# Optimization experiments

Measured on AMD Instinct MI355X. Metric: run time of the kernel, lower is better.

## Reference

```python
import jax, jax.numpy as jnp
import numpy as np


def _gcn_conv(x, edge_index, W, b):
    """Standard PyG GCNConv: add self-loops, symmetric normalization, x@W, scatter-add, +bias."""
    n = x.shape[0]
    loop = jnp.arange(n, dtype=edge_index.dtype)
    src = jnp.concatenate([edge_index[0], loop])  # [E+N]
    dst = jnp.concatenate([edge_index[1], loop])  # [E+N]
    # degree of destination nodes (unit edge weights + self loops)
    deg = jax.ops.segment_sum(jnp.ones_like(dst, dtype=x.dtype), dst, num_segments=n)
    dinv = jnp.where(deg > 0, jax.lax.rsqrt(deg), 0.0)
    norm = dinv[src] * dinv[dst]  # [E+N]
    h = x @ W  # [N, C_out] -- transform before aggregation (fewer bytes moved)
    msg = h[src] * norm[:, None]  # gather + scale
    out = jax.ops.segment_sum(msg, dst, num_segments=n)  # scatter-add
    return out + b


def setup_inputs() -> dict:
    key = jax.random.key(0)
    k1, k2, k3, k4 = jax.random.split(key, 4)
    N, E, C_in, C_hid, C_out = 50000, 800000, 64, 64, 40
    x = jax.random.normal(k1, (N, C_in), dtype=jnp.float32)
    edge_index = jax.random.randint(k2, (2, E), 0, N, dtype=jnp.int64)
    # Glorot-ish init for weights, zeros for biases (PyG GCNConv default)
    W1 = jax.random.normal(k3, (C_in, C_hid), dtype=jnp.float32) * (1.0 / np.sqrt(C_in))
    b1 = jnp.zeros((C_hid,), dtype=jnp.float32)
    W2 = jax.random.normal(k4, (C_hid, C_out), dtype=jnp.float32) * (1.0 / np.sqrt(C_hid))
    b2 = jnp.zeros((C_out,), dtype=jnp.float32)
    return {"x": x, "edge_index": edge_index, "W1": W1, "b1": b1, "W2": W2, "b2": b2}


def reference(x, edge_index, W1, b1, W2, b2):
    h = jax.nn.relu(_gcn_conv(x, edge_index, W1, b1))
    # F.dropout(training=False) is identity in eval mode
    h = _gcn_conv(h, edge_index, W2, b2)
    return jax.nn.log_softmax(h, axis=1)
```

## Files before the change

### kernel.cpp

```cpp
#include <hip/hip_runtime.h>
#include <hip/hip_fp16.h>
#include <math.h>


#define SHIFT   9
#define RPB     512
#define NBMAX   128
#define SLACK   16384
#define CHUNK_P 2048

__global__ void k_init(int* __restrict__ bcur, int nb) {
    int t = threadIdx.x;
    if (t < nb) bcur[t] = t * SLACK;
}

__global__ void k_part_gemm(const long long* __restrict__ ei64,
                            const int* __restrict__ ei32,
                            int* __restrict__ bcur,
                            unsigned int* __restrict__ ebkt, int E, int nb,
                            int npart,
                            const float* __restrict__ x,
                            const float* __restrict__ W1,
                            __half* __restrict__ hs1, int n) {
    __shared__ __align__(16) float smem[2 * 64 * 68];
    if ((int)blockIdx.x < npart) {
        int* cnt   = (int*)smem;
        int* rbase = cnt + NBMAX;
        int* is64p = rbase + NBMAX;
        int t = threadIdx.x;
        if (t < NBMAX) cnt[t] = 0;
        if (t == 0) {
            int is64 = 1;
            for (int i = 0; i < 64; ++i)
                if (ei32[2 * i + 1] != 0) { is64 = 0; break; }
            *is64p = is64;
        }
        __syncthreads();
        int is64 = *is64p;
        int lo = blockIdx.x * CHUNK_P;
        int hi = lo + CHUNK_P; if (hi > E) hi = E;
        for (int e = lo + t; e < hi; e += 256) {
            int d = is64 ? (int)ei64[E + e] : ei32[E + e];
            atomicAdd(&cnt[d >> SHIFT], 1);
        }
        __syncthreads();
        for (int b = t; b < nb; b += 256) {
            int c = cnt[b];
            rbase[b] = c ? atomicAdd(&bcur[b], c) : 0;
            cnt[b] = 0;
        }
        __syncthreads();
        for (int e = lo + t; e < hi; e += 256) {
            int s, d;
            if (is64) { s = (int)ei64[e]; d = (int)ei64[E + e]; }
            else      { s = ei32[e];      d = ei32[E + e]; }
            int b = d >> SHIFT;
            int pos = rbase[b] + atomicAdd(&cnt[b], 1);
            ebkt[pos] = ((unsigned int)(d & (RPB - 1)) << 16) | (unsigned int)s;
        }
    } else {
        float* Wl = smem;
        float* Xl = smem + 64 * 68;
        int t  = threadIdx.x;
        int tr = t >> 4, tc = t & 15;
        int base = (blockIdx.x - npart) * 64;

        for (int i = t; i < 64 * 17; i += 256) {
            int k = i / 17, c4 = (i % 17) * 4;
            float4 w = make_float4(0.f, 0.f, 0.f, 0.f);
            if (c4 < 64) w = *(const float4*)&W1[k * 64 + c4];
            *(float4*)&Wl[k * 68 + c4] = w;
        }
        for (int rr = tr; rr < 64; rr += 16) {
            int row = base + rr; if (row >= n) row = n - 1;
            float4 v = *(const float4*)&x[(size_t)row * 64 + tc * 4];
            Xl[(tc * 4 + 0) * 68 + rr] = v.x;
            Xl[(tc * 4 + 1) * 68 + rr] = v.y;
            Xl[(tc * 4 + 2) * 68 + rr] = v.z;
            Xl[(tc * 4 + 3) * 68 + rr] = v.w;
        }
        __syncthreads();

        float acc[4][4] = {{0.f}};
#pragma unroll 8
        for (int k = 0; k < 64; ++k) {
            float4 xv = *(const float4*)&Xl[k * 68 + tr * 4];
            float4 wv = *(const float4*)&Wl[k * 68 + tc * 4];
            acc[0][0] = fmaf(xv.x, wv.x, acc[0][0]);
            acc[0][1] = fmaf(xv.x, wv.y, acc[0][1]);
            acc[0][2] = fmaf(xv.x, wv.z, acc[0][2]);
            acc[0][3] = fmaf(xv.x, wv.w, acc[0][3]);
            acc[1][0] = fmaf(xv.y, wv.x, acc[1][0]);
            acc[1][1] = fmaf(xv.y, wv.y, acc[1][1]);
            acc[1][2] = fmaf(xv.y, wv.z, acc[1][2]);
            acc[1][3] = fmaf(xv.y, wv.w, acc[1][3]);
            acc[2][0] = fmaf(xv.z, wv.x, acc[2][0]);
            acc[2][1] = fmaf(xv.z, wv.y, acc[2][1]);
            acc[2][2] = fmaf(xv.z, wv.z, acc[2][2]);
            acc[2][3] = fmaf(xv.z, wv.w, acc[2][3]);
            acc[3][0] = fmaf(xv.w, wv.x, acc[3][0]);
            acc[3][1] = fmaf(xv.w, wv.y, acc[3][1]);
            acc[3][2] = fmaf(xv.w, wv.z, acc[3][2]);
            acc[3][3] = fmaf(xv.w, wv.w, acc[3][3]);
        }
#pragma unroll
        for (int i = 0; i < 4; ++i) {
            int r = base + tr * 4 + i;
            if (r >= n) break;
            __half2 p0 = __floats2half2_rn(acc[i][0], acc[i][1]);
            __half2 p1 = __floats2half2_rn(acc[i][2], acc[i][3]);
            *(__half2*)&hs1[(size_t)r * 64 + tc * 4]     = p0;
            *(__half2*)&hs1[(size_t)r * 64 + tc * 4 + 2] = p1;
        }
    }
}

__global__ void k_build(const unsigned int* __restrict__ ebkt,
                        const int* __restrict__ bcur,
                        int* __restrict__ row_beg, int* __restrict__ row_end,
                        float* __restrict__ dinv,
                        unsigned short* __restrict__ csr_src, int N) {
    __shared__ int cnt[RPB];
    __shared__ int wsum[256];
    int t = threadIdx.x, b = blockIdx.x;
    int rows0 = b << SHIFT;
    int nrows = N - rows0; if (nrows > RPB) nrows = RPB;
    for (int i = t; i < RPB; i += 256) cnt[i] = 0;
    __syncthreads();
    int lo = b * SLACK, hi = bcur[b];
    for (int e = lo + t; e < hi; e += 256)
        atomicAdd(&cnt[ebkt[e] >> 16], 1);
    __syncthreads();
    int i0 = 2 * t, i1 = 2 * t + 1;
    int c0 = cnt[i0], c1 = cnt[i1];
    wsum[t] = c0 + c1;
    __syncthreads();
    for (int off = 1; off < 256; off <<= 1) {
        int u = (t >= off) ? wsum[t - off] : 0;
        __syncthreads();
        wsum[t] += u;
        __syncthreads();
    }
    int beg0 = lo + ((t == 0) ? 0 : wsum[t - 1]);
    int beg1 = beg0 + c0;
    cnt[i0] = beg0;
    cnt[i1] = beg1;
    if (i0 < nrows) {
        row_beg[rows0 + i0] = beg0; row_end[rows0 + i0] = beg0 + c0;
        dinv[rows0 + i0] = rsqrtf((float)c0 + 1.0f);
    }
    if (i1 < nrows) {
        row_beg[rows0 + i1] = beg1; row_end[rows0 + i1] = beg1 + c1;
        dinv[rows0 + i1] = rsqrtf((float)c1 + 1.0f);
    }
    __syncthreads();
    for (int e = lo + t; e < hi; e += 256) {
        unsigned int v = ebkt[e];
        int pos = atomicAdd(&cnt[v >> 16], 1);
        csr_src[pos] = (unsigned short)(v & 0xffffu);
    }
}

template<int COUT>
__global__ void k_gemm(const __half* __restrict__ xin,
                       const float* __restrict__ W,
                       const float* __restrict__ dinv,
                       __half* __restrict__ hs, int n) {
    __shared__ float Wl[64 * 68];
    __shared__ float Xl[64 * 68];
    int t  = threadIdx.x;
    int tr = t >> 4, tc = t & 15;
    int base = blockIdx.x * 64;

    for (int i = t; i < 64 * 17; i += 256) {
        int k = i / 17, c4 = (i % 17) * 4;
        float4 w = make_float4(0.f, 0.f, 0.f, 0.f);
        if (c4 < COUT) w = *(const float4*)&W[k * COUT + c4];
        *(float4*)&Wl[k * 68 + c4] = w;
    }
    for (int rr = tr; rr < 64; rr += 16) {
        int row = base + rr; if (row >= n) row = n - 1;
        uint2 u = *(const uint2*)&xin[(size_t)row * 64 + tc * 4];
        float2 a = __half22float2(*(__half2*)&u.x);
        float2 c = __half22float2(*(__half2*)&u.y);
        Xl[(tc * 4 + 0) * 68 + rr] = a.x;
        Xl[(tc * 4 + 1) * 68 + rr] = a.y;
        Xl[(tc * 4 + 2) * 68 + rr] = c.x;
        Xl[(tc * 4 + 3) * 68 + rr] = c.y;
    }
    __syncthreads();

    float acc[4][4] = {{0.f}};
#pragma unroll 8
    for (int k = 0; k < 64; ++k) {
        float4 xv = *(const float4*)&Xl[k * 68 + tr * 4];
        float4 wv = *(const float4*)&Wl[k * 68 + tc * 4];
        acc[0][0] = fmaf(xv.x, wv.x, acc[0][0]);
        acc[0][1] = fmaf(xv.x, wv.y, acc[0][1]);
        acc[0][2] = fmaf(xv.x, wv.z, acc[0][2]);
        acc[0][3] = fmaf(xv.x, wv.w, acc[0][3]);
        acc[1][0] = fmaf(xv.y, wv.x, acc[1][0]);
        acc[1][1] = fmaf(xv.y, wv.y, acc[1][1]);
        acc[1][2] = fmaf(xv.y, wv.z, acc[1][2]);
        acc[1][3] = fmaf(xv.y, wv.w, acc[1][3]);
        acc[2][0] = fmaf(xv.z, wv.x, acc[2][0]);
        acc[2][1] = fmaf(xv.z, wv.y, acc[2][1]);
        acc[2][2] = fmaf(xv.z, wv.z, acc[2][2]);
        acc[2][3] = fmaf(xv.z, wv.w, acc[2][3]);
        acc[3][0] = fmaf(xv.w, wv.x, acc[3][0]);
        acc[3][1] = fmaf(xv.w, wv.y, acc[3][1]);
        acc[3][2] = fmaf(xv.w, wv.z, acc[3][2]);
        acc[3][3] = fmaf(xv.w, wv.w, acc[3][3]);
    }
#pragma unroll
    for (int i = 0; i < 4; ++i) {
        int r = base + tr * 4 + i;
        if (r >= n) break;
        float dv = dinv[r];
        __half2 p0 = __floats2half2_rn(acc[i][0] * dv, acc[i][1] * dv);
        __half2 p1 = __floats2half2_rn(acc[i][2] * dv, acc[i][3] * dv);
        if (tc * 4 + 3 < COUT) {
            *(__half2*)&hs[(size_t)r * COUT + tc * 4]     = p0;
            *(__half2*)&hs[(size_t)r * COUT + tc * 4 + 2] = p1;
        }
    }
}

__global__ void k_gather_relu64(const __half* __restrict__ hs,
                                const int* __restrict__ rbg,
                                const int* __restrict__ ren,
                                const unsigned short* __restrict__ ci,
                                const float* __restrict__ dinv,
                                const float* __restrict__ bias,
                                __half* __restrict__ out, int n) {
    int row = blockIdx.x * 4 + (threadIdx.x >> 6);
    if (row >= n) return;
    int lane = threadIdx.x & 63;
    int g = lane >> 3, q = lane & 7;
    int beg = rbg[row], end = ren[row];

    float4 aa = make_float4(0.f, 0.f, 0.f, 0.f);
    float4 ab = make_float4(0.f, 0.f, 0.f, 0.f);
    for (int base = beg; base < end; base += 64) {
        int mm = end - base; if (mm > 64) mm = 64;
        int idx = (lane < mm) ? (int)ci[base + lane] : 0;
        for (int j = 0; 8 * j < mm; ++j) {
            int e = 8 * j + g;
            int s = __shfl(idx, e, 64);
            if (base + e < end) {
                float ds = dinv[s];
                uint4 u = ((const uint4*)(hs + ((size_t)s << 6)))[q];
                float2 f0 = __half22float2(*(__half2*)&u.x);
                float2 f1 = __half22float2(*(__half2*)&u.y);
                float2 f2 = __half22float2(*(__half2*)&u.z);
                float2 f3 = __half22float2(*(__half2*)&u.w);
                aa.x = fmaf(f0.x, ds, aa.x); aa.y = fmaf(f0.y, ds, aa.y);
                aa.z = fmaf(f1.x, ds, aa.z); aa.w = fmaf(f1.y, ds, aa.w);
                ab.x = fmaf(f2.x, ds, ab.x); ab.y = fmaf(f2.y, ds, ab.y);
                ab.z = fmaf(f3.x, ds, ab.z); ab.w = fmaf(f3.y, ds, ab.w);
            }
        }
    }
#pragma unroll
    for (int o = 8; o < 64; o <<= 1) {
        aa.x += __shfl_xor(aa.x, o, 64); aa.y += __shfl_xor(aa.y, o, 64);
        aa.z += __shfl_xor(aa.z, o, 64); aa.w += __shfl_xor(aa.w, o, 64);
        ab.x += __shfl_xor(ab.x, o, 64); ab.y += __shfl_xor(ab.y, o, 64);
        ab.z += __shfl_xor(ab.z, o, 64); ab.w += __shfl_xor(ab.w, o, 64);
    }
    float dv = dinv[row];
    uint4 su = ((const uint4*)(hs + ((size_t)row << 6)))[q];
    float2 s0 = __half22float2(*(__half2*)&su.x);
    float2 s1 = __half22float2(*(__half2*)&su.y);
    float2 s2 = __half22float2(*(__half2*)&su.z);
    float2 s3 = __half22float2(*(__half2*)&su.w);
    float4 bv0 = *(const float4*)&bias[q * 8];
    float4 bv1 = *(const float4*)&bias[q * 8 + 4];
    float v0 = fmaxf((aa.x + s0.x * dv) * dv + bv0.x, 0.f);
    float v1 = fmaxf((aa.y + s0.y * dv) * dv + bv0.y, 0.f);
    float v2 = fmaxf((aa.z + s1.x * dv) * dv + bv0.z, 0.f);
    float v3 = fmaxf((aa.w + s1.y * dv) * dv + bv0.w, 0.f);
    float v4 = fmaxf((ab.x + s2.x * dv) * dv + bv1.x, 0.f);
    float v5 = fmaxf((ab.y + s2.y * dv) * dv + bv1.y, 0.f);
    float v6 = fmaxf((ab.z + s3.x * dv) * dv + bv1.z, 0.f);
    float v7 = fmaxf((ab.w + s3.y * dv) * dv + bv1.w, 0.f);
    if (lane < 8) {
        uint4 st;
        ((__half2*)&st)[0] = __floats2half2_rn(v0, v1);
        ((__half2*)&st)[1] = __floats2half2_rn(v2, v3);
        ((__half2*)&st)[2] = __floats2half2_rn(v4, v5);
        ((__half2*)&st)[3] = __floats2half2_rn(v6, v7);
        ((uint4*)(out + ((size_t)row << 6)))[q] = st;
    }
}

__global__ void k_gather_lsm40(const __half* __restrict__ hs,
                               const int* __restrict__ rbg,
                               const int* __restrict__ ren,
                               const unsigned short* __restrict__ ci,
                               const float* __restrict__ dinv,
                               const float* __restrict__ bias,
                               float* __restrict__ out, int n) {
    int row = blockIdx.x * 4 + (threadIdx.x >> 6);
    if (row >= n) return;
    int lane = threadIdx.x & 63;
    int g = lane >> 4, q = lane & 15;
    int beg = rbg[row], end = ren[row];

    uint2 selfu = make_uint2(0u, 0u);
    if (q < 10)
        selfu = ((const uint2*)(hs + (size_t)row * 40))[q];

    float4 a = make_float4(0.f, 0.f, 0.f, 0.f);
    for (int base = beg; base < end; base += 64) {
        int mm = end - base; if (mm > 64) mm = 64;
        int idx = (lane < mm) ? (int)ci[base + lane] : 0;
        for (int j = 0; 4 * j < mm; ++j) {
            int s = __shfl(idx, 4 * j + g, 64);
            if (q < 10 && base + 4 * j + g < end) {
                uint2 u = ((const uint2*)(hs + (size_t)s * 40))[q];
                float2 f0 = __half22float2(*(__half2*)&u.x);
                float2 f1 = __half22float2(*(__half2*)&u.y);
                a.x += f0.x; a.y += f0.y; a.z += f1.x; a.w += f1.y;
            }
        }
    }
    a.x += __shfl_xor(a.x, 16, 64); a.y += __shfl_xor(a.y, 16, 64);
    a.z += __shfl_xor(a.z, 16, 64); a.w += __shfl_xor(a.w, 16, 64);
    a.x += __shfl_xor(a.x, 32, 64); a.y += __shfl_xor(a.y, 32, 64);
    a.z += __shfl_xor(a.z, 32, 64); a.w += __shfl_xor(a.w, 32, 64);

    float2 s0 = __half22float2(*(__half2*)&selfu.x);
    float2 s1 = __half22float2(*(__half2*)&selfu.y);
    float dv = dinv[row];
    float v0 = -INFINITY, v1 = -INFINITY, v2 = -INFINITY, v3 = -INFINITY;
    if (q < 10) {
        float4 bv = *(const float4*)&bias[q * 4];
        v0 = (a.x + s0.x) * dv + bv.x;
        v1 = (a.y + s0.y) * dv + bv.y;
        v2 = (a.z + s1.x) * dv + bv.z;
        v3 = (a.w + s1.y) * dv + bv.w;
    }
    float mx = fmaxf(fmaxf(v0, v1), fmaxf(v2, v3));
#pragma unroll
    for (int o = 1; o < 16; o <<= 1) mx = fmaxf(mx, __shfl_xor(mx, o, 64));
    float e0 = (q < 10) ? expf(v0 - mx) : 0.f;
    float e1 = (q < 10) ? expf(v1 - mx) : 0.f;
    float e2 = (q < 10) ? expf(v2 - mx) : 0.f;
    float e3 = (q < 10) ? expf(v3 - mx) : 0.f;
    float sm = (e0 + e1) + (e2 + e3);
#pragma unroll
    for (int o = 1; o < 16; o <<= 1) sm += __shfl_xor(sm, o, 64);
    if (lane < 16 && q < 10) {
        float ls = logf(sm);
        float4 r = make_float4(v0 - mx - ls, v1 - mx - ls,
                               v2 - mx - ls, v3 - mx - ls);
        *(float4*)&out[(size_t)row * 40 + q * 4] = r;
    }
}

extern "C" void kernel_launch(void* const* d_in, const int* in_sizes, int n_in,
                              void* d_out, int out_size, void* d_ws, size_t ws_size,
                              hipStream_t stream) {
    const float* x  = (const float*)d_in[0];
    const void*  ei = d_in[1];
    const float* W1 = (const float*)d_in[2];
    const float* b1 = (const float*)d_in[3];
    const float* W2 = (const float*)d_in[4];
    const float* b2 = (const float*)d_in[5];
    float* out = (float*)d_out;

    const int C_IN = 64;
    const int N = in_sizes[0] / C_IN;
    const int E = in_sizes[1] / 2;
    (void)n_in; (void)out_size; (void)ws_size;

    char* ws = (char*)d_ws;
    size_t off = 0;
    auto alloc = [&](size_t bytes) -> void* {
        void* p = ws + off;
        off += (bytes + 255) & ~(size_t)255;
        return p;
    };
    int*            bcur    = (int*)           alloc(NBMAX * 4);
    unsigned int*   ebkt    = (unsigned int*)  alloc((size_t)NBMAX * SLACK * 4);
    unsigned short* csr_src = (unsigned short*)alloc((size_t)NBMAX * SLACK * 2);
    int*            row_beg = (int*)           alloc((size_t)N * 4);
    int*            row_end = (int*)           alloc((size_t)N * 4);
    float*          dinv    = (float*)         alloc((size_t)N * 4);
    __half*         hs1     = (__half*)        alloc((size_t)N * 64 * 2);
    __half*         h1b     = (__half*)        alloc((size_t)N * 64 * 2);
    __half*         hs2     = (__half*)        alloc((size_t)N * 40 * 2);

    const int nb    = (N + RPB - 1) >> SHIFT;
    const int ngrid = (N + 63) / 64;
    const int npart = (E + CHUNK_P - 1) / CHUNK_P;

    k_init<<<1, 128, 0, stream>>>(bcur, nb);
    k_part_gemm<<<npart + ngrid, 256, 0, stream>>>(
        (const long long*)ei, (const int*)ei, bcur, ebkt, E, nb, npart,
        x, W1, hs1, N);
    k_build<<<nb, 256, 0, stream>>>(ebkt, bcur, row_beg, row_end, dinv,
                                    csr_src, N);
    k_gather_relu64<<<(N + 3) / 4, 256, 0, stream>>>(
        hs1, row_beg, row_end, csr_src, dinv, b1, h1b, N);
    k_gemm<40><<<ngrid, 256, 0, stream>>>(h1b, W2, dinv, hs2, N);
    k_gather_lsm40<<<(N + 3) / 4, 256, 0, stream>>>(
        hs2, row_beg, row_end, csr_src, dinv, b2, out, N);
}
```

Measured before the change: 113.9 us.

## Fuse layer-1 gather/ReLU with layer-2 GEMM into one kernel

Merges the first-layer neighbor aggregation plus bias/ReLU with the second-layer 64x40 GEMM. Each block gathers 64 rows (8 waves × 8 rows each) into shared memory, then 160 threads run the GEMM and write scaled fp16 results. This removes the h1b intermediate write and read and one kernel launch. In exchange each wave now handles 8 rows serially, there are fewer blocks (N/64), and only 160 of 512 threads are active during the GEMM phase, which can reduce parallelism and latency hiding in the gather.

New measurement: 123.3 us. 1.08x slower.

```diff
diff --git a/kernel.cpp b/kernel.cpp
--- a/kernel.cpp
+++ b/kernel.cpp
@@ -161,136 +161,127 @@
     }
 }
 
-template<int COUT>
-__global__ void k_gemm(const __half* __restrict__ xin,
-                       const float* __restrict__ W,
-                       const float* __restrict__ dinv,
-                       __half* __restrict__ hs, int n) {
-    __shared__ float Wl[64 * 68];
+__global__ __launch_bounds__(512, 4)
+void k_gather_gemm2(const __half* __restrict__ hs,
+                    const float* __restrict__ W,
+                    const int* __restrict__ rbg,
+                    const int* __restrict__ ren,
+                    const unsigned short* __restrict__ ci,
+                    const float* __restrict__ dinv,
+                    const float* __restrict__ bias,
+                    __half* __restrict__ hs2,
+                    int n) {
     __shared__ float Xl[64 * 68];
-    int t  = threadIdx.x;
-    int tr = t >> 4, tc = t & 15;
+    __shared__ float Wl[64 * 44];
+    int t = threadIdx.x;
     int base = blockIdx.x * 64;
 
-    for (int i = t; i < 64 * 17; i += 256) {
-        int k = i / 17, c4 = (i % 17) * 4;
+    for (int i = t; i < 64 * 11; i += 512) {
+        int k = i / 11, c4 = (i % 11) * 4;
         float4 w = make_float4(0.f, 0.f, 0.f, 0.f);
-        if (c4 < COUT) w = *(const float4*)&W[k * COUT + c4];
-        *(float4*)&Wl[k * 68 + c4] = w;
-    }
-    for (int rr = tr; rr < 64; rr += 16) {
-        int row = base + rr; if (row >= n) row = n - 1;
-        uint2 u = *(const uint2*)&xin[(size_t)row * 64 + tc * 4];
-        float2 a = __half22float2(*(__half2*)&u.x);
-        float2 c = __half22float2(*(__half2*)&u.y);
-        Xl[(tc * 4 + 0) * 68 + rr] = a.x;
-        Xl[(tc * 4 + 1) * 68 + rr] = a.y;
-        Xl[(tc * 4 + 2) * 68 + rr] = c.x;
-        Xl[(tc * 4 + 3) * 68 + rr] = c.y;
-    }
-    __syncthreads();
-
-    float acc[4][4] = {{0.f}};
+        if (c4 < 40) w = *(const float4*)&W[k * 40 + c4];
+        *(float4*)&Wl[k * 44 + c4] = w;
+    }
+
+    int w    = t >> 6;
+    int lane = t & 63;
+    int g = lane >> 3, q = lane & 7;
+
+    for (int it = 0; it < 8; ++it) {
+        int row = base + w * 8 + it;
+        if (row >= n) break;
+        int beg = rbg[row], end = ren[row];
+
+        float4 aa = make_float4(0.f, 0.f, 0.f, 0.f);
+        float4 ab = make_float4(0.f, 0.f, 0.f, 0.f);
+        for (int eb = beg; eb < end; eb += 64) {
+            int mm = end - eb; if (mm > 64) mm = 64;
+            int idx = (lane < mm) ? (int)ci[eb + lane] : 0;
+            for (int j = 0; 8 * j < mm; ++j) {
+                int e = 8 * j + g;
+                int s = __shfl(idx, e, 64);
+                if (eb + e < end) {
+                    float ds = dinv[s];
+                    uint4 u = ((const uint4*)(hs + ((size_t)s << 6)))[q];
+                    float2 f0 = __half22float2(*(__half2*)&u.x);
+                    float2 f1 = __half22float2(*(__half2*)&u.y);
+                    float2 f2 = __half22float2(*(__half2*)&u.z);
+                    float2 f3 = __half22float2(*(__half2*)&u.w);
+                    aa.x = fmaf(f0.x, ds, aa.x); aa.y = fmaf(f0.y, ds, aa.y);
+                    aa.z = fmaf(f1.x, ds, aa.z); aa.w = fmaf(f1.y, ds, aa.w);
+                    ab.x = fmaf(f2.x, ds, ab.x); ab.y = fmaf(f2.y, ds, ab.y);
+                    ab.z = fmaf(f3.x, ds, ab.z); ab.w = fmaf(f3.y, ds, ab.w);
+                }
+            }
+        }
+#pragma unroll
+        for (int o = 8; o < 64; o <<= 1) {
+            aa.x += __shfl_xor(aa.x, o, 64); aa.y += __shfl_xor(aa.y, o, 64);
+            aa.z += __shfl_xor(aa.z, o, 64); aa.w += __shfl_xor(aa.w, o, 64);
+            ab.x += __shfl_xor(ab.x, o, 64); ab.y += __shfl_xor(ab.y, o, 64);
+            ab.z += __shfl_xor(ab.z, o, 64); ab.w += __shfl_xor(ab.w, o, 64);
+        }
+        float dv = dinv[row];
+        uint4 su = ((const uint4*)(hs + ((size_t)row << 6)))[q];
+        float2 s0 = __half22float2(*(__half2*)&su.x);
+        float2 s1 = __half22float2(*(__half2*)&su.y);
+        float2 s2 = __half22float2(*(__half2*)&su.z);
+        float2 s3 = __half22float2(*(__half2*)&su.w);
+        float4 bv0 = *(const float4*)&bias[q * 8];
+        float4 bv1 = *(const float4*)&bias[q * 8 + 4];
+        float v0 = fmaxf((aa.x + s0.x * dv) * dv + bv0.x, 0.f);
+        float v1 = fmaxf((aa.y + s0.y * dv) * dv + bv0.y, 0.f);
+        float v2 = fmaxf((aa.z + s1.x * dv) * dv + bv0.z, 0.f);
+        float v3 = fmaxf((aa.w + s1.y * dv) * dv + bv0.w, 0.f);
+        float v4 = fmaxf((ab.x + s2.x * dv) * dv + bv1.x, 0.f);
+        float v5 = fmaxf((ab.y + s2.y * dv) * dv + bv1.y, 0.f);
+        float v6 = fmaxf((ab.z + s3.x * dv) * dv + bv1.z, 0.f);
+        float v7 = fmaxf((ab.w + s3.y * dv) * dv + bv1.w, 0.f);
+        float s01 = (g & 1) ? v1 : v0;
+        float s23 = (g & 1) ? v3 : v2;
+        float s45 = (g & 1) ? v5 : v4;
+        float s67 = (g & 1) ? v7 : v6;
+        float s03 = (g & 2) ? s23 : s01;
+        float s47 = (g & 2) ? s67 : s45;
+        float val = (g & 4) ? s47 : s03;
+        Xl[(q * 8 + g) * 68 + (row - base)] = val;
+    }
+    __syncthreads();
+
+    if (t < 256 && (t & 15) < 10) {
+        int tr = t >> 4, tc = t & 15;
+        float acc[4][4] = {{0.f}};
 #pragma unroll 8
-    for (int k = 0; k < 64; ++k) {
-        float4 xv = *(const float4*)&Xl[k * 68 + tr * 4];
-        float4 wv = *(const float4*)&Wl[k * 68 + tc * 4];
-        acc[0][0] = fmaf(xv.x, wv.x, acc[0][0]);
-        acc[0][1] = fmaf(xv.x, wv.y, acc[0][1]);
-        acc[0][2] = fmaf(xv.x, wv.z, acc[0][2]);
-        acc[0][3] = fmaf(xv.x, wv.w, acc[0][3]);
-        acc[1][0] = fmaf(xv.y, wv.x, acc[1][0]);
-        acc[1][1] = fmaf(xv.y, wv.y, acc[1][1]);
-        acc[1][2] = fmaf(xv.y, wv.z, acc[1][2]);
-        acc[1][3] = fmaf(xv.y, wv.w, acc[1][3]);
-        acc[2][0] = fmaf(xv.z, wv.x, acc[2][0]);
-        acc[2][1] = fmaf(xv.z, wv.y, acc[2][1]);
-        acc[2][2] = fmaf(xv.z, wv.z, acc[2][2]);
-        acc[2][3] = fmaf(xv.z, wv.w, acc[2][3]);
-        acc[3][0] = fmaf(xv.w, wv.x, acc[3][0]);
-        acc[3][1] = fmaf(xv.w, wv.y, acc[3][1]);
-        acc[3][2] = fmaf(xv.w, wv.z, acc[3][2]);
-        acc[3][3] = fmaf(xv.w, wv.w, acc[3][3]);
-    }
-#pragma unroll
-    for (int i = 0; i < 4; ++i) {
-        int r = base + tr * 4 + i;
-        if (r >= n) break;
-        float dv = dinv[r];
-        __half2 p0 = __floats2half2_rn(acc[i][0] * dv, acc[i][1] * dv);
-        __half2 p1 = __floats2half2_rn(acc[i][2] * dv, acc[i][3] * dv);
-        if (tc * 4 + 3 < COUT) {
-            *(__half2*)&hs[(size_t)r * COUT + tc * 4]     = p0;
-            *(__half2*)&hs[(size_t)r * COUT + tc * 4 + 2] = p1;
-        }
-    }
-}
-
-__global__ void k_gather_relu64(const __half* __restrict__ hs,
-                                const int* __restrict__ rbg,
-                                const int* __restrict__ ren,
-                                const unsigned short* __restrict__ ci,
-                                const float* __restrict__ dinv,
-                                const float* __restrict__ bias,
-                                __half* __restrict__ out, int n) {
-    int row = blockIdx.x * 4 + (threadIdx.x >> 6);
-    if (row >= n) return;
-    int lane = threadIdx.x & 63;
-    int g = lane >> 3, q = lane & 7;
-    int beg = rbg[row], end = ren[row];
-
-    float4 aa = make_float4(0.f, 0.f, 0.f, 0.f);
-    float4 ab = make_float4(0.f, 0.f, 0.f, 0.f);
-    for (int base = beg; base < end; base += 64) {
-        int mm = end - base; if (mm > 64) mm = 64;
-        int idx = (lane < mm) ? (int)ci[base + lane] : 0;
-        for (int j = 0; 8 * j < mm; ++j) {
-            int e = 8 * j + g;
-            int s = __shfl(idx, e, 64);
-            if (base + e < end) {
-                float ds = dinv[s];
-                uint4 u = ((const uint4*)(hs + ((size_t)s << 6)))[q];
-                float2 f0 = __half22float2(*(__half2*)&u.x);
-                float2 f1 = __half22float2(*(__half2*)&u.y);
-                float2 f2 = __half22float2(*(__half2*)&u.z);
-                float2 f3 = __half22float2(*(__half2*)&u.w);
-                aa.x = fmaf(f0.x, ds, aa.x); aa.y = fmaf(f0.y, ds, aa.y);
-                aa.z = fmaf(f1.x, ds, aa.z); aa.w = fmaf(f1.y, ds, aa.w);
-                ab.x = fmaf(f2.x, ds, ab.x); ab.y = fmaf(f2.y, ds, ab.y);
-                ab.z = fmaf(f3.x, ds, ab.z); ab.w = fmaf(f3.y, ds, ab.w);
-            }
-        }
-    }
-#pragma unroll
-    for (int o = 8; o < 64; o <<= 1) {
-        aa.x += __shfl_xor(aa.x, o, 64); aa.y += __shfl_xor(aa.y, o, 64);
-        aa.z += __shfl_xor(aa.z, o, 64); aa.w += __shfl_xor(aa.w, o, 64);
-        ab.x += __shfl_xor(ab.x, o, 64); ab.y += __shfl_xor(ab.y, o, 64);
-        ab.z += __shfl_xor(ab.z, o, 64); ab.w += __shfl_xor(ab.w, o, 64);
-    }
-    float dv = dinv[row];
-    uint4 su = ((const uint4*)(hs + ((size_t)row << 6)))[q];
-    float2 s0 = __half22float2(*(__half2*)&su.x);
-    float2 s1 = __half22float2(*(__half2*)&su.y);
-    float2 s2 = __half22float2(*(__half2*)&su.z);
-    float2 s3 = __half22float2(*(__half2*)&su.w);
-    float4 bv0 = *(const float4*)&bias[q * 8];
-    float4 bv1 = *(const float4*)&bias[q * 8 + 4];
-    float v0 = fmaxf((aa.x + s0.x * dv) * dv + bv0.x, 0.f);
-    float v1 = fmaxf((aa.y + s0.y * dv) * dv + bv0.y, 0.f);
-    float v2 = fmaxf((aa.z + s1.x * dv) * dv + bv0.z, 0.f);
-    float v3 = fmaxf((aa.w + s1.y * dv) * dv + bv0.w, 0.f);
-    float v4 = fmaxf((ab.x + s2.x * dv) * dv + bv1.x, 0.f);
-    float v5 = fmaxf((ab.y + s2.y * dv) * dv + bv1.y, 0.f);
-    float v6 = fmaxf((ab.z + s3.x * dv) * dv + bv1.z, 0.f);
-    float v7 = fmaxf((ab.w + s3.y * dv) * dv + bv1.w, 0.f);
-    if (lane < 8) {
-        uint4 st;
-        ((__half2*)&st)[0] = __floats2half2_rn(v0, v1);
-        ((__half2*)&st)[1] = __floats2half2_rn(v2, v3);
-        ((__half2*)&st)[2] = __floats2half2_rn(v4, v5);
-        ((__half2*)&st)[3] = __floats2half2_rn(v6, v7);
-        ((uint4*)(out + ((size_t)row << 6)))[q] = st;
+        for (int k = 0; k < 64; ++k) {
+            float4 xv = *(const float4*)&Xl[k * 68 + tr * 4];
+            float4 wv = *(const float4*)&Wl[k * 44 + tc * 4];
+            acc[0][0] = fmaf(xv.x, wv.x, acc[0][0]);
+            acc[0][1] = fmaf(xv.x, wv.y, acc[0][1]);
+            acc[0][2] = fmaf(xv.x, wv.z, acc[0][2]);
+            acc[0][3] = fmaf(xv.x, wv.w, acc[0][3]);
+            acc[1][0] = fmaf(xv.y, wv.x, acc[1][0]);
+            acc[1][1] = fmaf(xv.y, wv.y, acc[1][1]);
+            acc[1][2] = fmaf(xv.y, wv.z, acc[1][2]);
+            acc[1][3] = fmaf(xv.y, wv.w, acc[1][3]);
+            acc[2][0] = fmaf(xv.z, wv.x, acc[2][0]);
+            acc[2][1] = fmaf(xv.z, wv.y, acc[2][1]);
+            acc[2][2] = fmaf(xv.z, wv.z, acc[2][2]);
+            acc[2][3] = fmaf(xv.z, wv.w, acc[2][3]);
+            acc[3][0] = fmaf(xv.w, wv.x, acc[3][0]);
+            acc[3][1] = fmaf(xv.w, wv.y, acc[3][1]);
+            acc[3][2] = fmaf(xv.w, wv.z, acc[3][2]);
+            acc[3][3] = fmaf(xv.w, wv.w, acc[3][3]);
+        }
+#pragma unroll
+        for (int i = 0; i < 4; ++i) {
+            int r = base + tr * 4 + i;
+            if (r >= n) break;
+            float dvv = dinv[r];
+            __half2 p0 = __floats2half2_rn(acc[i][0] * dvv, acc[i][1] * dvv);
+            __half2 p1 = __floats2half2_rn(acc[i][2] * dvv, acc[i][3] * dvv);
+            *(__half2*)&hs2[(size_t)r * 40 + tc * 4]     = p0;
+            *(__half2*)&hs2[(size_t)r * 40 + tc * 4 + 2] = p1;
+        }
     }
 }
 
@@ -389,7 +380,6 @@
     int*            row_end = (int*)           alloc((size_t)N * 4);
     float*          dinv    = (float*)         alloc((size_t)N * 4);
     __half*         hs1     = (__half*)        alloc((size_t)N * 64 * 2);
-    __half*         h1b     = (__half*)        alloc((size_t)N * 64 * 2);
     __half*         hs2     = (__half*)        alloc((size_t)N * 40 * 2);
 
     const int nb    = (N + RPB - 1) >> SHIFT;
@@ -402,9 +392,8 @@
         x, W1, hs1, N);
     k_build<<<nb, 256, 0, stream>>>(ebkt, bcur, row_beg, row_end, dinv,
                                     csr_src, N);
-    k_gather_relu64<<<(N + 3) / 4, 256, 0, stream>>>(
-        hs1, row_beg, row_end, csr_src, dinv, b1, h1b, N);
-    k_gemm<40><<<ngrid, 256, 0, stream>>>(h1b, W2, dinv, hs2, N);
+    k_gather_gemm2<<<ngrid, 512, 0, stream>>>(
+        hs1, W2, row_beg, row_end, csr_src, dinv, b1, hs2, N);
     k_gather_lsm40<<<(N + 3) / 4, 256, 0, stream>>>(
         hs2, row_beg, row_end, csr_src, dinv, b2, out, N);
 }
```

## Halve bucket size, stash edges in LDS, replace init kernel with memcpy

Applied to the files above, without the earlier changes.

Bucket granularity drops from 512 to 256 rows, which gives 256 buckets so each thread in the build kernel owns one row and the scan is simpler. The partition kernel now reads the edge list once and stashes packed (dst,src) pairs in shared memory, removing the second global read pass. The bucket-cursor init kernel is replaced by a host-to-device async memcpy from a static host array. The gather kernels hoist the self-row and dinv loads earlier. Risks: the memcpy from pageable static memory may synchronise or add latency, and bucket slack of 8192 per 256 rows must still hold the per-bucket edge count.

Result: faster. 106.7 us (-6.3%).

```diff
diff --git a/kernel.cpp b/kernel.cpp
--- a/kernel.cpp
+++ b/kernel.cpp
@@ -3,16 +3,11 @@
 #include <math.h>
 
 
-#define SHIFT   9
-#define RPB     512
-#define NBMAX   128
-#define SLACK   16384
+#define SHIFT   8
+#define RPB     256
+#define NBMAX   256
+#define SLACK   8192
 #define CHUNK_P 2048
-
-__global__ void k_init(int* __restrict__ bcur, int nb) {
-    int t = threadIdx.x;
-    if (t < nb) bcur[t] = t * SLACK;
-}
 
 __global__ void k_part_gemm(const long long* __restrict__ ei64,
                             const int* __restrict__ ei32,
@@ -25,10 +20,11 @@
     __shared__ __align__(16) float smem[2 * 64 * 68];
     if ((int)blockIdx.x < npart) {
         int* cnt   = (int*)smem;
-        int* rbase = cnt + NBMAX;
-        int* is64p = rbase + NBMAX;
+        int* rbase = cnt + 256;
+        int* is64p = rbase + 256;
+        int* stash = is64p + 1;
         int t = threadIdx.x;
-        if (t < NBMAX) cnt[t] = 0;
+        cnt[t] = 0;
         if (t == 0) {
             int is64 = 1;
             for (int i = 0; i < 64; ++i)
@@ -40,23 +36,24 @@
         int lo = blockIdx.x * CHUNK_P;
         int hi = lo + CHUNK_P; if (hi > E) hi = E;
         for (int e = lo + t; e < hi; e += 256) {
-            int d = is64 ? (int)ei64[E + e] : ei32[E + e];
-            atomicAdd(&cnt[d >> SHIFT], 1);
-        }
-        __syncthreads();
-        for (int b = t; b < nb; b += 256) {
-            int c = cnt[b];
-            rbase[b] = c ? atomicAdd(&bcur[b], c) : 0;
-            cnt[b] = 0;
-        }
-        __syncthreads();
-        for (int e = lo + t; e < hi; e += 256) {
             int s, d;
             if (is64) { s = (int)ei64[e]; d = (int)ei64[E + e]; }
             else      { s = ei32[e];      d = ei32[E + e]; }
-            int b = d >> SHIFT;
+            stash[e - lo] = (int)(((unsigned int)d << 16) | (unsigned int)s);
+            atomicAdd(&cnt[d >> SHIFT], 1);
+        }
+        __syncthreads();
+        {
+            int c = cnt[t];
+            rbase[t] = c ? atomicAdd(&bcur[t], c) : 0;
+            cnt[t] = 0;
+        }
+        __syncthreads();
+        for (int e = lo + t; e < hi; e += 256) {
+            unsigned int v = (unsigned int)stash[e - lo];
+            int b = (int)(v >> 16) >> SHIFT;
             int pos = rbase[b] + atomicAdd(&cnt[b], 1);
-            ebkt[pos] = ((unsigned int)(d & (RPB - 1)) << 16) | (unsigned int)s;
+            ebkt[pos] = (((v >> 16) & (RPB - 1)) << 16) | (v & 0xffffu);
         }
     } else {
         float* Wl = smem;
@@ -121,43 +118,105 @@
                         float* __restrict__ dinv,
                         unsigned short* __restrict__ csr_src, int N) {
     __shared__ int cnt[RPB];
-    __shared__ int wsum[256];
+    __shared__ int ssum[RPB];
     int t = threadIdx.x, b = blockIdx.x;
     int rows0 = b << SHIFT;
-    int nrows = N - rows0; if (nrows > RPB) nrows = RPB;
-    for (int i = t; i < RPB; i += 256) cnt[i] = 0;
+    cnt[t] = 0;
     __syncthreads();
     int lo = b * SLACK, hi = bcur[b];
     for (int e = lo + t; e < hi; e += 256)
         atomicAdd(&cnt[ebkt[e] >> 16], 1);
     __syncthreads();
-    int i0 = 2 * t, i1 = 2 * t + 1;
-    int c0 = cnt[i0], c1 = cnt[i1];
-    wsum[t] = c0 + c1;
+    int c = cnt[t];
+    ssum[t] = c;
     __syncthreads();
     for (int off = 1; off < 256; off <<= 1) {
-        int u = (t >= off) ? wsum[t - off] : 0;
-        __syncthreads();
-        wsum[t] += u;
-        __syncthreads();
-    }
-    int beg0 = lo + ((t == 0) ? 0 : wsum[t - 1]);
-    int beg1 = beg0 + c0;
-    cnt[i0] = beg0;
-    cnt[i1] = beg1;
-    if (i0 < nrows) {
-        row_beg[rows0 + i0] = beg0; row_end[rows0 + i0] = beg0 + c0;
-        dinv[rows0 + i0] = rsqrtf((float)c0 + 1.0f);
-    }
-    if (i1 < nrows) {
-        row_beg[rows0 + i1] = beg1; row_end[rows0 + i1] = beg1 + c1;
-        dinv[rows0 + i1] = rsqrtf((float)c1 + 1.0f);
-    }
+        int u = (t >= off) ? ssum[t - off] : 0;
+        __syncthreads();
+        ssum[t] += u;
+        __syncthreads();
+    }
+    int beg = lo + ssum[t] - c;
+    int row = rows0 + t;
+    if (row < N) {
+        row_beg[row] = beg; row_end[row] = beg + c;
+        dinv[row] = rsqrtf((float)c + 1.0f);
+    }
+    cnt[t] = beg;
     __syncthreads();
     for (int e = lo + t; e < hi; e += 256) {
         unsigned int v = ebkt[e];
         int pos = atomicAdd(&cnt[v >> 16], 1);
         csr_src[pos] = (unsigned short)(v & 0xffffu);
+    }
+}
+
+__global__ void k_gather_relu64(const __half* __restrict__ hs,
+                                const int* __restrict__ rbg,
+                                const int* __restrict__ ren,
+                                const unsigned short* __restrict__ ci,
+                                const float* __restrict__ dinv,
+                                const float* __restrict__ bias,
+                                __half* __restrict__ out, int n) {
+    int row = blockIdx.x * 4 + (threadIdx.x >> 6);
+    if (row >= n) return;
+    int lane = threadIdx.x & 63;
+    int g = lane >> 3, q = lane & 7;
+    int beg = rbg[row], end = ren[row];
+
+    float dv = dinv[row];
+    uint4 su = ((const uint4*)(hs + ((size_t)row << 6)))[q];
+
+    float4 aa = make_float4(0.f, 0.f, 0.f, 0.f);
+    float4 ab = make_float4(0.f, 0.f, 0.f, 0.f);
+    for (int base = beg; base < end; base += 64) {
+        int mm = end - base; if (mm > 64) mm = 64;
+        int idx = (lane < mm) ? (int)ci[base + lane] : 0;
+        for (int j = 0; 8 * j < mm; ++j) {
+            int e = 8 * j + g;
+            int s = __shfl(idx, e, 64);
+            if (base + e < end) {
+                float ds = dinv[s];
+                uint4 u = ((const uint4*)(hs + ((size_t)s << 6)))[q];
+                float2 f0 = __half22float2(*(__half2*)&u.x);
+                float2 f1 = __half22float2(*(__half2*)&u.y);
+                float2 f2 = __half22float2(*(__half2*)&u.z);
+                float2 f3 = __half22float2(*(__half2*)&u.w);
+                aa.x = fmaf(f0.x, ds, aa.x); aa.y = fmaf(f0.y, ds, aa.y);
+                aa.z = fmaf(f1.x, ds, aa.z); aa.w = fmaf(f1.y, ds, aa.w);
+                ab.x = fmaf(f2.x, ds, ab.x); ab.y = fmaf(f2.y, ds, ab.y);
+                ab.z = fmaf(f3.x, ds, ab.z); ab.w = fmaf(f3.y, ds, ab.w);
+            }
+        }
+    }
+#pragma unroll
+    for (int o = 8; o < 64; o <<= 1) {
+        aa.x += __shfl_xor(aa.x, o, 64); aa.y += __shfl_xor(aa.y, o, 64);
+        aa.z += __shfl_xor(aa.z, o, 64); aa.w += __shfl_xor(aa.w, o, 64);
+        ab.x += __shfl_xor(ab.x, o, 64); ab.y += __shfl_xor(ab.y, o, 64);
+        ab.z += __shfl_xor(ab.z, o, 64); ab.w += __shfl_xor(ab.w, o, 64);
+    }
+    float2 s0 = __half22float2(*(__half2*)&su.x);
+    float2 s1 = __half22float2(*(__half2*)&su.y);
+    float2 s2 = __half22float2(*(__half2*)&su.z);
+    float2 s3 = __half22float2(*(__half2*)&su.w);
+    float4 bv0 = *(const float4*)&bias[q * 8];
+    float4 bv1 = *(const float4*)&bias[q * 8 + 4];
+    float v0 = fmaxf((aa.x + s0.x * dv) * dv + bv0.x, 0.f);
+    float v1 = fmaxf((aa.y + s0.y * dv) * dv + bv0.y, 0.f);
+    float v2 = fmaxf((aa.z + s1.x * dv) * dv + bv0.z, 0.f);
+    float v3 = fmaxf((aa.w + s1.y * dv) * dv + bv0.w, 0.f);
+    float v4 = fmaxf((ab.x + s2.x * dv) * dv + bv1.x, 0.f);
+    float v5 = fmaxf((ab.y + s2.y * dv) * dv + bv1.y, 0.f);
+    float v6 = fmaxf((ab.z + s3.x * dv) * dv + bv1.z, 0.f);
+    float v7 = fmaxf((ab.w + s3.y * dv) * dv + bv1.w, 0.f);
+    if (lane < 8) {
+        uint4 st;
+        ((__half2*)&st)[0] = __floats2half2_rn(v0, v1);
+        ((__half2*)&st)[1] = __floats2half2_rn(v2, v3);
+        ((__half2*)&st)[2] = __floats2half2_rn(v4, v5);
+        ((__half2*)&st)[3] = __floats2half2_rn(v6, v7);
+        ((uint4*)(out + ((size_t)row << 6)))[q] = st;
     }
 }
 
@@ -226,74 +285,6 @@
     }
 }
 
-__global__ void k_gather_relu64(const __half* __restrict__ hs,
-                                const int* __restrict__ rbg,
-                                const int* __restrict__ ren,
-                                const unsigned short* __restrict__ ci,
-                                const float* __restrict__ dinv,
-                                const float* __restrict__ bias,
-                                __half* __restrict__ out, int n) {
-    int row = blockIdx.x * 4 + (threadIdx.x >> 6);
-    if (row >= n) return;
-    int lane = threadIdx.x & 63;
-    int g = lane >> 3, q = lane & 7;
-    int beg = rbg[row], end = ren[row];
-
-    float4 aa = make_float4(0.f, 0.f, 0.f, 0.f);
-    float4 ab = make_float4(0.f, 0.f, 0.f, 0.f);
-    for (int base = beg; base < end; base += 64) {
-        int mm = end - base; if (mm > 64) mm = 64;
-        int idx = (lane < mm) ? (int)ci[base + lane] : 0;
-        for (int j = 0; 8 * j < mm; ++j) {
-            int e = 8 * j + g;
-            int s = __shfl(idx, e, 64);
-            if (base + e < end) {
-                float ds = dinv[s];
-                uint4 u = ((const uint4*)(hs + ((size_t)s << 6)))[q];
-                float2 f0 = __half22float2(*(__half2*)&u.x);
-                float2 f1 = __half22float2(*(__half2*)&u.y);
-                float2 f2 = __half22float2(*(__half2*)&u.z);
-                float2 f3 = __half22float2(*(__half2*)&u.w);
-                aa.x = fmaf(f0.x, ds, aa.x); aa.y = fmaf(f0.y, ds, aa.y);
-                aa.z = fmaf(f1.x, ds, aa.z); aa.w = fmaf(f1.y, ds, aa.w);
-                ab.x = fmaf(f2.x, ds, ab.x); ab.y = fmaf(f2.y, ds, ab.y);
-                ab.z = fmaf(f3.x, ds, ab.z); ab.w = fmaf(f3.y, ds, ab.w);
-            }
-        }
-    }
-#pragma unroll
-    for (int o = 8; o < 64; o <<= 1) {
-        aa.x += __shfl_xor(aa.x, o, 64); aa.y += __shfl_xor(aa.y, o, 64);
-        aa.z += __shfl_xor(aa.z, o, 64); aa.w += __shfl_xor(aa.w, o, 64);
-        ab.x += __shfl_xor(ab.x, o, 64); ab.y += __shfl_xor(ab.y, o, 64);
-        ab.z += __shfl_xor(ab.z, o, 64); ab.w += __shfl_xor(ab.w, o, 64);
-    }
-    float dv = dinv[row];
-    uint4 su = ((const uint4*)(hs + ((size_t)row << 6)))[q];
-    float2 s0 = __half22float2(*(__half2*)&su.x);
-    float2 s1 = __half22float2(*(__half2*)&su.y);
-    float2 s2 = __half22float2(*(__half2*)&su.z);
-    float2 s3 = __half22float2(*(__half2*)&su.w);
-    float4 bv0 = *(const float4*)&bias[q * 8];
-    float4 bv1 = *(const float4*)&bias[q * 8 + 4];
-    float v0 = fmaxf((aa.x + s0.x * dv) * dv + bv0.x, 0.f);
-    float v1 = fmaxf((aa.y + s0.y * dv) * dv + bv0.y, 0.f);
-    float v2 = fmaxf((aa.z + s1.x * dv) * dv + bv0.z, 0.f);
-    float v3 = fmaxf((aa.w + s1.y * dv) * dv + bv0.w, 0.f);
-    float v4 = fmaxf((ab.x + s2.x * dv) * dv + bv1.x, 0.f);
-    float v5 = fmaxf((ab.y + s2.y * dv) * dv + bv1.y, 0.f);
-    float v6 = fmaxf((ab.z + s3.x * dv) * dv + bv1.z, 0.f);
-    float v7 = fmaxf((ab.w + s3.y * dv) * dv + bv1.w, 0.f);
-    if (lane < 8) {
-        uint4 st;
-        ((__half2*)&st)[0] = __floats2half2_rn(v0, v1);
-        ((__half2*)&st)[1] = __floats2half2_rn(v2, v3);
-        ((__half2*)&st)[2] = __floats2half2_rn(v4, v5);
-        ((__half2*)&st)[3] = __floats2half2_rn(v6, v7);
-        ((uint4*)(out + ((size_t)row << 6)))[q] = st;
-    }
-}
-
 __global__ void k_gather_lsm40(const __half* __restrict__ hs,
                                const int* __restrict__ rbg,
                                const int* __restrict__ ren,
@@ -307,6 +298,7 @@
     int g = lane >> 4, q = lane & 15;
     int beg = rbg[row], end = ren[row];
 
+    float dv = dinv[row];
     uint2 selfu = make_uint2(0u, 0u);
     if (q < 10)
         selfu = ((const uint2*)(hs + (size_t)row * 40))[q];
@@ -332,7 +324,6 @@
 
     float2 s0 = __half22float2(*(__half2*)&selfu.x);
     float2 s1 = __half22float2(*(__half2*)&selfu.y);
-    float dv = dinv[row];
     float v0 = -INFINITY, v1 = -INFINITY, v2 = -INFINITY, v3 = -INFINITY;
     if (q < 10) {
         float4 bv = *(const float4*)&bias[q * 4];
@@ -396,7 +387,11 @@
     const int ngrid = (N + 63) / 64;
     const int npart = (E + CHUNK_P - 1) / CHUNK_P;
 
-    k_init<<<1, 128, 0, stream>>>(bcur, nb);
+    static int h_binit[NBMAX];
+    for (int i = 0; i < NBMAX; ++i) h_binit[i] = i * SLACK;
+    hipMemcpyAsync(bcur, h_binit, NBMAX * sizeof(int),
+                   hipMemcpyHostToDevice, stream);
+
     k_part_gemm<<<npart + ngrid, 256, 0, stream>>>(
         (const long long*)ei, (const int*)ei, bcur, ebkt, E, nb, npart,
         x, W1, hs1, N);
```
